# Optimization experiments

Measured on AMD Instinct MI355X. Metric: run time of the kernel, lower is better.

## Reference

```python
import jax, jax.numpy as jnp
import numpy as np

B, F, T = 256, 64, 1024  # batch, num_frequencies, trailing columns; state dim = 2F = 128


def setup_inputs() -> dict:
    key = jax.random.key(0)
    k1, k2, k3, k4 = jax.random.split(key, 4)
    x = jax.random.normal(k1, (B, 2 * F, T), dtype=jnp.float32)
    # positive dts so amp**dt and 2*pi/|dt| in the repo are well-behaved
    delta_t = jax.random.uniform(k2, (B,), dtype=jnp.float32, minval=0.5, maxval=2.0)
    # learned params: amplitudes init'd to 1.0, frequencies ~ U(0, 2*pi) in the torch code;
    # perturb amplitudes slightly so the amp**dt path is exercised
    amplitudes = jax.random.uniform(k3, (F,), dtype=jnp.float32, minval=0.7, maxval=1.3)
    frequencies = jax.random.uniform(k4, (F,), dtype=jnp.float32, minval=0.0, maxval=2.0 * np.pi)
    return {"x": x, "delta_t": delta_t, "amplitudes": amplitudes, "frequencies": frequencies}


def reference(x, delta_t, amplitudes, frequencies):
    # Per-sample Jordan rotation matrix is block-diagonal with 2x2 blocks
    #   a^dt * [[cos(w*dt), -sin(w*dt)], [sin(w*dt), cos(w*dt)]]
    # Apply blocks directly instead of materializing the sparse [2F,2F] matrix.
    Bn = x.shape[0]
    Fn = amplitudes.shape[0]
    a = amplitudes[None, :] ** delta_t[:, None]          # [B, F]
    ang = frequencies[None, :] * delta_t[:, None]        # [B, F]
    c = a * jnp.cos(ang)                                 # [B, F]
    s = a * jnp.sin(ang)                                 # [B, F]
    xr = x.reshape(Bn, Fn, 2, -1)                        # [B, F, 2, T]
    x0, x1 = xr[:, :, 0], xr[:, :, 1]                    # [B, F, T]
    out0 = c[..., None] * x0 - s[..., None] * x1
    out1 = s[..., None] * x0 + c[..., None] * x1
    return jnp.stack([out0, out1], axis=2).reshape(x.shape)
```

## Files before the change

### kernel.cpp

```cpp
#include <hip/hip_runtime.h>


constexpr int Bn = 256;
constexpr int Fn = 64;
constexpr int Tn = 1024;
constexpr int ITERS = 8;
constexpr int GRID  = Bn * Fn / ITERS;

typedef float v4f __attribute__((ext_vector_type(4)));

__global__ __launch_bounds__(256) void koopman_kernel(
    const float* __restrict__ x,
    const float* __restrict__ delta_t,
    const float* __restrict__ amplitudes,
    const float* __restrict__ frequencies,
    float* __restrict__ out) {
    const int t      = threadIdx.x;
    const int bfBase = blockIdx.x * ITERS;

    const v4f* __restrict__ xp = reinterpret_cast<const v4f*>(x)
                               + (size_t)bfBase * 512;
    v4f*       __restrict__ op = reinterpret_cast<v4f*>(out)
                               + (size_t)bfBase * 512;

    v4f a0 = xp[t];
    v4f a1 = xp[t + 256];

#pragma unroll 2
    for (int j = 0; j < ITERS; ++j) {
        v4f n0, n1;
        if (j + 1 < ITERS) {
            n0 = xp[(j + 1) * 512 + t];
            n1 = xp[(j + 1) * 512 + 256 + t];
        }

        const int bf = bfBase + j;
        const int b  = bf >> 6;
        const int f  = bf & 63;
        const float d = delta_t[b];
        const float a = __builtin_amdgcn_exp2f(d * __builtin_amdgcn_logf(amplitudes[f]));
        const float rev = (frequencies[f] * d) * 0.15915494309189535f;
        const float s = a * __builtin_amdgcn_sinf(rev);
        const float c = a * __builtin_amdgcn_cosf(rev);

        const v4f r0 = c * a0 - s * a1;
        const v4f r1 = s * a0 + c * a1;
        __builtin_nontemporal_store(r0, &op[j * 512 + t]);
        __builtin_nontemporal_store(r1, &op[j * 512 + 256 + t]);

        a0 = n0;
        a1 = n1;
    }
}

extern "C" void kernel_launch(void* const* d_in, const int* in_sizes, int n_in,
                              void* d_out, int out_size, void* d_ws, size_t ws_size,
                              hipStream_t stream) {
    const float* x    = (const float*)d_in[0];
    const float* dt   = (const float*)d_in[1];
    const float* amp  = (const float*)d_in[2];
    const float* freq = (const float*)d_in[3];
    float* out = (float*)d_out;

    static_assert((Bn * Fn) % ITERS == 0, "grid divisibility");
    koopman_kernel<<<dim3(GRID), dim3(256), 0, stream>>>(x, dt, amp, freq, out);
}
```

Before: 239.1 us.

## Use persistent-style 256-block grid with 4-deep register prefetch ring

Shrinks the grid from 2048 blocks to 256 blocks, so each block now handles 64 (b,f) rows instead of 8. A 4-deep register ring buffer of loads replaces the single-step prefetch, keeping more memory requests in flight per thread. The aim is to cut block launch overhead and hide more latency in this bandwidth-bound rotation. The cost is that only 256 blocks cover 256 CUs with one wave group each, so occupancy and memory-level parallelism per CU may be too low to saturate HBM.

```diff
diff --git a/kernel.cpp b/kernel.cpp
--- a/kernel.cpp
+++ b/kernel.cpp
@@ -4,8 +4,9 @@
 constexpr int Bn = 256;
 constexpr int Fn = 64;
 constexpr int Tn = 1024;
-constexpr int ITERS = 8;
-constexpr int GRID  = Bn * Fn / ITERS;
+constexpr int BLOCKS = 256;
+constexpr int ITERS  = Bn * Fn / BLOCKS;
+constexpr int DEPTH  = 4;
 
 typedef float v4f __attribute__((ext_vector_type(4)));
 
@@ -23,15 +24,22 @@
     v4f*       __restrict__ op = reinterpret_cast<v4f*>(out)
                                + (size_t)bfBase * 512;
 
-    v4f a0 = xp[t];
-    v4f a1 = xp[t + 256];
+    v4f p0[DEPTH], p1[DEPTH];
+#pragma unroll
+    for (int j = 0; j < DEPTH; ++j) {
+        p0[j] = xp[j * 512 + t];
+        p1[j] = xp[j * 512 + 256 + t];
+    }
 
-#pragma unroll 2
+#pragma unroll 4
     for (int j = 0; j < ITERS; ++j) {
-        v4f n0, n1;
-        if (j + 1 < ITERS) {
-            n0 = xp[(j + 1) * 512 + t];
-            n1 = xp[(j + 1) * 512 + 256 + t];
+        const int sl = j & (DEPTH - 1);
+        const v4f d0 = p0[sl];
+        const v4f d1 = p1[sl];
+
+        if (j + DEPTH < ITERS) {
+            p0[sl] = xp[(j + DEPTH) * 512 + t];
+            p1[sl] = xp[(j + DEPTH) * 512 + 256 + t];
         }
 
         const int bf = bfBase + j;
@@ -43,13 +51,10 @@
         const float s = a * __builtin_amdgcn_sinf(rev);
         const float c = a * __builtin_amdgcn_cosf(rev);
 
-        const v4f r0 = c * a0 - s * a1;
-        const v4f r1 = s * a0 + c * a1;
+        const v4f r0 = c * d0 - s * d1;
+        const v4f r1 = s * d0 + c * d1;
         __builtin_nontemporal_store(r0, &op[j * 512 + t]);
         __builtin_nontemporal_store(r1, &op[j * 512 + 256 + t]);
-
-        a0 = n0;
-        a1 = n1;
     }
 }
 
@@ -62,6 +67,6 @@
     const float* freq = (const float*)d_in[3];
     float* out = (float*)d_out;
 
-    static_assert((Bn * Fn) % ITERS == 0, "grid divisibility");
-    koopman_kernel<<<dim3(GRID), dim3(256), 0, stream>>>(x, dt, amp, freq, out);
+    static_assert((Bn * Fn) % BLOCKS == 0, "grid divisibility");
+    koopman_kernel<<<dim3(BLOCKS), dim3(256), 0, stream>>>(x, dt, amp, freq, out);
 }
```

Measured after the change: 244.3 us. +2.2%, slower.
